# Kernel optimization log

Hardware: AMD Instinct MI355X
Metric: run time of the kernel (lower is better)

Reference implementation:

```python
import jax, jax.numpy as jnp
import numpy as np

E = 16       # num_experts
TOP_K = 2
D = 1024     # emb_dim
H = 1024     # moe_hidden_dim
SH = 2048    # shared_expert_hidden_dim
B, S = 2, 2048
W_SCALE = 0.02  # realistic init scale for weights


def setup_inputs() -> dict:
    key = jax.random.key(0)
    ks = jax.random.split(key, 9)
    return {
        "x": jax.random.normal(ks[0], (B, S, D), jnp.float32),
        "gate_w": jax.random.normal(ks[1], (E, D), jnp.float32) * W_SCALE,
        "w_gate": jax.random.normal(ks[2], (E, H, D), jnp.float32) * W_SCALE,
        "w1": jax.random.normal(ks[3], (E, H, D), jnp.float32) * W_SCALE,
        "w2": jax.random.normal(ks[4], (E, D, H), jnp.float32) * W_SCALE,
        "shared_w_gate": jax.random.normal(ks[5], (SH, D), jnp.float32) * W_SCALE,
        "shared_w1": jax.random.normal(ks[6], (SH, D), jnp.float32) * W_SCALE,
        "shared_w2": jax.random.normal(ks[7], (D, SH), jnp.float32) * W_SCALE,
        "shared_gate_w": jax.random.normal(ks[8], (1, D), jnp.float32) * W_SCALE,
    }


def reference(x, gate_w, w_gate, w1, w2, shared_w_gate, shared_w1, shared_w2, shared_gate_w):
    b, s, d = x.shape
    x2d = x.reshape(-1, d)                       # [N, D]
    n = x2d.shape[0]

    # --- router ---
    logits = x2d @ gate_w.T                      # [N, E]
    probs = jax.nn.softmax(logits, axis=-1)
    topk_p, topk_i = jax.lax.top_k(probs, TOP_K)  # [N, K]
    topk_p = topk_p / jnp.sum(topk_p, axis=-1, keepdims=True)

    # combine weights per (token, expert): zero for non-selected experts
    comb = jnp.zeros((n, E), x2d.dtype).at[jnp.arange(n)[:, None], topk_i].add(topk_p)  # [N, E]

    # --- per-expert gated FFN, accumulated via scan (keeps peak memory at [N,H]) ---
    def step(acc, ws):
        wg, wa, wo, cw = ws                      # [H,D], [H,D], [D,H], [N]
        h = (x2d @ wa.T) * jax.nn.silu(x2d @ wg.T)   # [N, H]
        return acc + cw[:, None] * (h @ wo.T), None

    out, _ = jax.lax.scan(step, jnp.zeros_like(x2d), (w_gate, w1, w2, comb.T))

    # --- shared expert path ---
    sh = (x2d @ shared_w1.T) * jax.nn.silu(x2d @ shared_w_gate.T)  # [N, SH]
    shared_out = sh @ shared_w2.T                                  # [N, D]
    sg = jax.nn.sigmoid(x2d @ shared_gate_w.T)                     # [N, 1]
    out = out + sg * shared_out

    return out.reshape(b, s, d)
```

## Files before the change

### kernel.cpp

```cpp
#include <hip/hip_runtime.h>
#include <stdint.h>

#define E_    16
#define TOPK  2
#define D_    1024
#define H_    1024
#define SH_   2048
#define NTOK  4096
#define BK    32
#define NDESC 80
#define RTOK  16
#define NRBLK (NTOK / RTOK)
#define NSHUP (NTOK/128 * SH_/128)
#define NRTUP (NDESC * H_/128)
#define NSHDN (NTOK/128 * D_/128)
#define NRTDN (NDESC * D_/128)

typedef unsigned short u16;
typedef __attribute__((ext_vector_type(8))) __bf16 bf16x8;
typedef __attribute__((ext_vector_type(4))) float  f32x4;

struct CvtTable {
  const float* src[7];
  u16*         dst[7];
  int          start[8];
};

__device__ __forceinline__ u16 f2bf(float f) {
  union { float f; unsigned int u; } v; v.f = f;
  unsigned int u = v.u;
  return (u16)((u + 0x7fffu + ((u >> 16) & 1u)) >> 16);
}

__device__ __forceinline__ void gload16(const void* g, void* l) {
  __builtin_amdgcn_global_load_lds(
      (const __attribute__((address_space(1))) unsigned int*)g,
      (__attribute__((address_space(3))) unsigned int*)l, 16, 0, 0);
}

__device__ __forceinline__ int swz8(int b, int nb) {
  return (b & 7) * (nb >> 3) + (b >> 3);
}

__global__ __launch_bounds__(256) void cvtrouter_k(
    CvtTable ct,
    const float* __restrict__ x, const float* __restrict__ gate_w,
    const float* __restrict__ shared_gate_w,
    int* __restrict__ topk_e, float* __restrict__ topk_w,
    float* __restrict__ sg, int* __restrict__ counts) {
  __shared__ float xs[RTOK][132];
  __shared__ float lg[RTOK][16];
  __shared__ float sgp[RTOK][16];

  int b   = blockIdx.x;
  int tid = threadIdx.x;

  if (b >= NRBLK) {
    int cb = b - NRBLK;
    int s = 0;
    while (cb >= ct.start[s + 1]) s++;
    int i = (cb - ct.start[s]) * 256 + tid;
    float4 f = ((const float4*)ct.src[s])[i];
    ushort4 o; o.x = f2bf(f.x); o.y = f2bf(f.y); o.z = f2bf(f.z); o.w = f2bf(f.w);
    ((ushort4*)ct.dst[s])[i] = o;
    return;
  }

  int e   = tid >> 4;
  int tt  = tid & 15;
  int t0  = b * RTOK;

  float acc = 0.f, sga = 0.f;
  for (int c = 0; c < D_; c += 128) {
    __syncthreads();
    #pragma unroll
    for (int i = 0; i < 2; i++) {
      int f = i * 256 + tid;
      int r = f >> 5, c4 = f & 31;
      *(float4*)&xs[r][c4 * 4] =
          *(const float4*)&x[(size_t)(t0 + r) * D_ + c + c4 * 4];
    }
    __syncthreads();
    const float* gw = &gate_w[(size_t)e * D_ + c];
    #pragma unroll
    for (int d4 = 0; d4 < 32; d4++) {
      float4 g  = *(const float4*)&gw[d4 * 4];
      float4 xv = *(const float4*)&xs[tt][d4 * 4];
      acc += xv.x * g.x + xv.y * g.y + xv.z * g.z + xv.w * g.w;
    }
    #pragma unroll
    for (int j = 0; j < 8; j += 4) {
      float4 s2 = *(const float4*)&shared_gate_w[c + e * 8 + j];
      float4 xv = *(const float4*)&xs[tt][e * 8 + j];
      sga += xv.x * s2.x + xv.y * s2.y + xv.z * s2.z + xv.w * s2.w;
    }
  }
  lg[tt][e]  = acc;
  sgp[tt][e] = sga;
  __syncthreads();

  if (tid < RTOK) {
    int t = t0 + tid;
    float l[16];
    #pragma unroll
    for (int k = 0; k < 16; k++) l[k] = lg[tid][k];
    int i0 = 0; float l0 = l[0];
    for (int k = 1; k < 16; k++) if (l[k] > l0) { l0 = l[k]; i0 = k; }
    int i1 = -1; float l1 = -3.4e38f;
    for (int k = 0; k < 16; k++) if (k != i0 && l[k] > l1) { l1 = l[k]; i1 = k; }
    float w0 = 1.f / (1.f + expf(l1 - l0));
    float s = 0.f;
    #pragma unroll
    for (int k = 0; k < 16; k++) s += sgp[tid][k];
    topk_e[2*t] = i0; topk_e[2*t+1] = i1;
    topk_w[2*t] = w0; topk_w[2*t+1] = 1.f - w0;
    sg[t] = 1.f / (1.f + expf(-s));
    atomicAdd(&counts[i0], 1);
    atomicAdd(&counts[i1], 1);
  }
}

__global__ __launch_bounds__(256) void scan_scatter_k(
    const int* __restrict__ counts, int* __restrict__ offs,
    int* __restrict__ desc_e, int* __restrict__ desc_m,
    const int* __restrict__ topk_e, const float* __restrict__ topk_w,
    int* __restrict__ fill, int* __restrict__ tok_of, float* __restrict__ w_of) {
  if (threadIdx.x == 0) {
    int s = 0, n = 0;
    for (int e = 0; e < E_; e++) {
      offs[e] = s;
      for (int m0 = 0; m0 < counts[e]; m0 += 128) {
        desc_e[n] = e; desc_m[n] = m0; n++;
      }
      s += counts[e];
    }
    offs[E_] = s;
    for (; n < NDESC; n++) { desc_e[n] = -1; desc_m[n] = 0; }
  }
  __syncthreads();
  for (int t = threadIdx.x; t < NTOK; t += 256) {
    for (int k = 0; k < TOPK; k++) {
      int e = topk_e[2*t+k];
      int p = atomicAdd(&fill[e], 1);
      int slot = offs[e] + p;
      tok_of[slot] = t;
      w_of[slot]   = topk_w[2*t+k];
    }
  }
}

__global__ __launch_bounds__(256, 2) void up_merged(
    const u16* __restrict__ Xb,
    const u16* __restrict__ sWg, const u16* __restrict__ sW1, u16* __restrict__ sHout,
    const u16* __restrict__ rWg_all, const u16* __restrict__ rW1_all, u16* __restrict__ rHout,
    const int* __restrict__ tok_of,
    const int* __restrict__ offs, const int* __restrict__ counts,
    const int* __restrict__ desc_e, const int* __restrict__ desc_m) {
  int bid = blockIdx.x;
  const u16 *Wg, *W1; u16* Hout; int Hdim;
  int m0, cnt, pbase, n0;
  const int* tof;
  if (bid < NSHUP) {
    int l = swz8(bid, NSHUP);
    int bx = l >> 4, by = l & 15;
    m0 = bx * 128; cnt = NTOK; pbase = 0; tof = nullptr;
    Wg = sWg; W1 = sW1; Hout = sHout; Hdim = SH_;
    n0 = by * 128;
  } else {
    int r = bid - NSHUP;
    int l = swz8(r, NRTUP);
    int bx = l >> 3, by = l & 7;
    int e = desc_e[bx];
    if (e < 0) return;
    m0 = desc_m[bx]; cnt = counts[e]; pbase = offs[e]; tof = tok_of;
    Wg = rWg_all + (size_t)e * H_ * D_;
    W1 = rW1_all + (size_t)e * H_ * D_;
    Hout = rHout; Hdim = H_;
    n0 = by * 128;
  }

  __shared__ u16 smem[2 * 3 * 4096];

  int tid  = threadIdx.x;
  int lane = tid & 63, wave = tid >> 6;
  int wm = wave & 1, wn = wave >> 1;
  int l16 = lane & 15, quad = lane >> 4;

  int sr = wave * 16 + (lane >> 2);
  int sc = (lane & 3) * 8;

  int gm0 = m0 + sr;      if (gm0 >= cnt) gm0 = cnt - 1;
  int gm1 = m0 + sr + 64; if (gm1 >= cnt) gm1 = cnt - 1;
  int tok0 = tof ? tof[pbase + gm0] : gm0;
  int tok1 = tof ? tof[pbase + gm1] : gm1;
  const u16* pa0 = Xb + (size_t)tok0 * D_ + sc;
  const u16* pa1 = Xb + (size_t)tok1 * D_ + sc;
  const u16* pg0 = Wg + (size_t)(n0 + sr) * D_ + sc;
  const u16* pg1 = pg0 + (size_t)64 * D_;
  const u16* pu0 = W1 + (size_t)(n0 + sr) * D_ + sc;
  const u16* pu1 = pu0 + (size_t)64 * D_;

  int lbase = wave * 512;

  f32x4 accg[4][4], accu[4][4];
  f32x4 zero = {0.f, 0.f, 0.f, 0.f};
  #pragma unroll
  for (int i = 0; i < 4; i++)
    #pragma unroll
    for (int j = 0; j < 4; j++) { accg[i][j] = zero; accu[i][j] = zero; }

#define STAGE_UP(b) do {                                            \
    u16* s_ = smem + (b) * 12288 + lbase;                           \
    gload16(pa0, s_);        gload16(pa1, s_ + 2048);               \
    gload16(pg0, s_ + 4096); gload16(pg1, s_ + 6144);               \
    gload16(pu0, s_ + 8192); gload16(pu1, s_ + 10240);              \
    pa0 += BK; pa1 += BK; pg0 += BK; pg1 += BK; pu0 += BK; pu1 += BK; \
  } while (0)

  STAGE_UP(0);
  STAGE_UP(1);
  int buf = 0;
  const int nt = D_ / BK;

  for (int t = 0; t < nt; ++t) {
    if (t + 1 < nt) asm volatile("s_waitcnt vmcnt(6)" ::: "memory");
    else            asm volatile("s_waitcnt vmcnt(0)" ::: "memory");
    __builtin_amdgcn_s_barrier();
    __builtin_amdgcn_sched_barrier(0);

    const u16* base = smem + buf * 12288;
    bf16x8 af[4], gf[4], uf[4];
    #pragma unroll
    for (int i = 0; i < 4; i++) {
      af[i] = *(const bf16x8*)&base[(wm*64 + i*16 + l16)*BK + quad*8];
      gf[i] = *(const bf16x8*)&base[4096 + (wn*64 + i*16 + l16)*BK + quad*8];
      uf[i] = *(const bf16x8*)&base[8192 + (wn*64 + i*16 + l16)*BK + quad*8];
    }
    #pragma unroll
    for (int i = 0; i < 4; i++)
      #pragma unroll
      for (int j = 0; j < 4; j++) {
        accg[i][j] = __builtin_amdgcn_mfma_f32_16x16x32_bf16(af[i], gf[j], accg[i][j], 0, 0, 0);
        accu[i][j] = __builtin_amdgcn_mfma_f32_16x16x32_bf16(af[i], uf[j], accu[i][j], 0, 0, 0);
      }

    __builtin_amdgcn_sched_barrier(0);
    __builtin_amdgcn_s_barrier();
    if (t + 2 < nt) STAGE_UP(buf);
    buf ^= 1;
  }
#undef STAGE_UP

  #pragma unroll
  for (int i = 0; i < 4; i++) {
    #pragma unroll
    for (int r = 0; r < 4; r++) {
      int m = m0 + wm*64 + i*16 + quad*4 + r;
      if (m < cnt) {
        size_t prow = (size_t)(pbase + m) * Hdim;
        #pragma unroll
        for (int j = 0; j < 4; j++) {
          int n = n0 + wn*64 + j*16 + l16;
          float g = accg[i][j][r];
          float u = accu[i][j][r];
          Hout[prow + n] = f2bf(u * (g / (1.f + expf(-g))));
        }
      }
    }
  }
}

__global__ __launch_bounds__(256, 3) void down_merged(
    const u16* __restrict__ sHbuf, const u16* __restrict__ sW2, const float* __restrict__ sg,
    const u16* __restrict__ rHbuf, const u16* __restrict__ rW2_all, const float* __restrict__ w_of,
    float* __restrict__ out,
    const int* __restrict__ tok_of,
    const int* __restrict__ offs, const int* __restrict__ counts,
    const int* __restrict__ desc_e, const int* __restrict__ desc_m) {
  int bid = blockIdx.x;
  const u16 *Hbuf, *W2; const float* scale;
  int m0, cnt, pbase, n0, K;
  const int* tof;
  if (bid < NSHDN) {
    int l = swz8(bid, NSHDN);
    int bx = l >> 3, by = l & 7;
    m0 = bx * 128; cnt = NTOK; pbase = 0; tof = nullptr;
    Hbuf = sHbuf; W2 = sW2; scale = sg; K = SH_;
    n0 = by * 128;
  } else {
    int r = bid - NSHDN;
    int l = swz8(r, NRTDN);
    int bx = l >> 3, by = l & 7;
    int e = desc_e[bx];
    if (e < 0) return;
    m0 = desc_m[bx]; cnt = counts[e]; pbase = offs[e]; tof = tok_of;
    Hbuf = rHbuf; W2 = rW2_all + (size_t)e * D_ * H_; scale = w_of; K = H_;
    n0 = by * 128;
  }

  __shared__ u16 smem[2 * 2 * 4096];

  int tid  = threadIdx.x;
  int lane = tid & 63, wave = tid >> 6;
  int wm = wave & 1, wn = wave >> 1;
  int l16 = lane & 15, quad = lane >> 4;

  int sr = wave * 16 + (lane >> 2);
  int sc = (lane & 3) * 8;

  int gm0 = m0 + sr;      if (gm0 >= cnt) gm0 = cnt - 1;
  int gm1 = m0 + sr + 64; if (gm1 >= cnt) gm1 = cnt - 1;
  const u16* pa0 = Hbuf + (size_t)(pbase + gm0) * K + sc;
  const u16* pa1 = Hbuf + (size_t)(pbase + gm1) * K + sc;
  const u16* pb0 = W2 + (size_t)(n0 + sr) * K + sc;
  const u16* pb1 = pb0 + (size_t)64 * K;

  int lbase = wave * 512;

  f32x4 acc[4][4];
  f32x4 zero = {0.f, 0.f, 0.f, 0.f};
  #pragma unroll
  for (int i = 0; i < 4; i++)
    #pragma unroll
    for (int j = 0; j < 4; j++) acc[i][j] = zero;

#define STAGE_DN(b) do {                                \
    u16* s_ = smem + (b) * 8192 + lbase;                \
    gload16(pa0, s_);        gload16(pa1, s_ + 2048);   \
    gload16(pb0, s_ + 4096); gload16(pb1, s_ + 6144);   \
    pa0 += BK; pa1 += BK; pb0 += BK; pb1 += BK;         \
  } while (0)

  STAGE_DN(0);
  STAGE_DN(1);
  int buf = 0;
  const int nt = K / BK;

  for (int t = 0; t < nt; ++t) {
    if (t + 1 < nt) asm volatile("s_waitcnt vmcnt(4)" ::: "memory");
    else            asm volatile("s_waitcnt vmcnt(0)" ::: "memory");
    __builtin_amdgcn_s_barrier();
    __builtin_amdgcn_sched_barrier(0);

    const u16* base = smem + buf * 8192;
    bf16x8 af[4], bfr[4];
    #pragma unroll
    for (int i = 0; i < 4; i++) {
      af[i]  = *(const bf16x8*)&base[(wm*64 + i*16 + l16)*BK + quad*8];
      bfr[i] = *(const bf16x8*)&base[4096 + (wn*64 + i*16 + l16)*BK + quad*8];
    }
    #pragma unroll
    for (int i = 0; i < 4; i++)
      #pragma unroll
      for (int j = 0; j < 4; j++)
        acc[i][j] = __builtin_amdgcn_mfma_f32_16x16x32_bf16(af[i], bfr[j], acc[i][j], 0, 0, 0);

    __builtin_amdgcn_sched_barrier(0);
    __builtin_amdgcn_s_barrier();
    if (t + 2 < nt) STAGE_DN(buf);
    buf ^= 1;
  }
#undef STAGE_DN

  #pragma unroll
  for (int i = 0; i < 4; i++) {
    #pragma unroll
    for (int r = 0; r < 4; r++) {
      int m = m0 + wm*64 + i*16 + quad*4 + r;
      if (m < cnt) {
        int p   = pbase + m;
        int tok = tof ? tof[p] : p;
        float sc2 = scale[p];
        #pragma unroll
        for (int j = 0; j < 4; j++) {
          int n = n0 + wn*64 + j*16 + l16;
          atomicAdd(&out[(size_t)tok * D_ + n], sc2 * acc[i][j][r]);
        }
      }
    }
  }
}

extern "C" void kernel_launch(void* const* d_in, const int* in_sizes, int n_in,
                              void* d_out, int out_size, void* d_ws, size_t ws_size,
                              hipStream_t stream) {
  const float* x      = (const float*)d_in[0];
  const float* gate_w = (const float*)d_in[1];
  const float* w_gate = (const float*)d_in[2];
  const float* w1     = (const float*)d_in[3];
  const float* w2     = (const float*)d_in[4];
  const float* sh_wg  = (const float*)d_in[5];
  const float* sh_w1  = (const float*)d_in[6];
  const float* sh_w2  = (const float*)d_in[7];
  const float* sh_gw  = (const float*)d_in[8];
  float* out = (float*)d_out;

  char* ws = (char*)d_ws;
  size_t off = 0;
  u16* xb    = (u16*)(ws + off); off += (size_t)NTOK * D_ * 2;
  u16* h_exp = (u16*)(ws + off); off += (size_t)NTOK * TOPK * H_ * 2;
  u16* h_sh  = (u16*)(ws + off); off += (size_t)NTOK * SH_ * 2;
  u16* wb_g  = (u16*)(ws + off); off += (size_t)E_ * H_ * D_ * 2;
  u16* wb_1  = (u16*)(ws + off); off += (size_t)E_ * H_ * D_ * 2;
  u16* wb_2  = (u16*)(ws + off); off += (size_t)E_ * D_ * H_ * 2;
  u16* sb_g  = (u16*)(ws + off); off += (size_t)SH_ * D_ * 2;
  u16* sb_1  = (u16*)(ws + off); off += (size_t)SH_ * D_ * 2;
  u16* sb_2  = (u16*)(ws + off); off += (size_t)D_ * SH_ * 2;
  int*   tok_of = (int*)  (ws + off); off += NTOK * TOPK * 4;
  float* w_of   = (float*)(ws + off); off += NTOK * TOPK * 4;
  float* sg     = (float*)(ws + off); off += NTOK * 4;
  int*   topk_e = (int*)  (ws + off); off += NTOK * TOPK * 4;
  float* topk_w = (float*)(ws + off); off += NTOK * TOPK * 4;
  int*   counts = (int*)  (ws + off); off += 64;
  int*   offs   = (int*)  (ws + off); off += 128;
  int*   fill   = (int*)  (ws + off); off += 64;
  int*   desc_e = (int*)  (ws + off); off += NDESC * 4;
  int*   desc_m = (int*)  (ws + off); off += NDESC * 4;

  hipMemsetAsync(counts, 0, 256, stream);
  hipMemsetAsync(out, 0, (size_t)NTOK * D_ * 4, stream);

  CvtTable ct;
  const float* srcs[7] = {x, w_gate, w1, w2, sh_wg, sh_w1, sh_w2};
  u16*         dsts[7] = {xb, wb_g, wb_1, wb_2, sb_g, sb_1, sb_2};
  int          nblk[7] = {NTOK*D_/1024, E_*H_*D_/1024, E_*H_*D_/1024,
                          E_*D_*H_/1024, SH_*D_/1024, SH_*D_/1024, D_*SH_/1024};
  int s = 0;
  for (int i = 0; i < 7; i++) { ct.src[i] = srcs[i]; ct.dst[i] = dsts[i];
                                ct.start[i] = s; s += nblk[i]; }
  ct.start[7] = s;

  cvtrouter_k<<<dim3(NRBLK + s), 256, 0, stream>>>(
      ct, x, gate_w, sh_gw, topk_e, topk_w, sg, counts);
  scan_scatter_k<<<dim3(1), 256, 0, stream>>>(
      counts, offs, desc_e, desc_m, topk_e, topk_w, fill, tok_of, w_of);

  up_merged<<<dim3(NSHUP + NRTUP), 256, 0, stream>>>(
      xb, sb_g, sb_1, h_sh, wb_g, wb_1, h_exp,
      tok_of, offs, counts, desc_e, desc_m);
  down_merged<<<dim3(NSHDN + NRTDN), 256, 0, stream>>>(
      h_sh, sb_2, sg, h_exp, wb_2, w_of, out,
      tok_of, offs, counts, desc_e, desc_m);

  (void)in_sizes; (void)n_in; (void)ws_size;
}
```

Baseline: 464.6 us.

## Defer down-proj weight conversion into up GEMM grid; atomic-free scatter

Moves the fp32-to-bf16 conversion of w2 and shared_w2 out of the first kernel and into extra tail blocks of the up-projection launch. The conversion then runs alongside the up GEMM instead of sitting on the critical path before it. Separately, replaces the global atomic counters and fill counters with a per-thread shared-memory histogram and prefix scan inside the single-block scatter kernel, which also removes the counts memset. The risk is that the conversion blocks compete with GEMM blocks for bandwidth and CUs, and that the scan serializes work on 16 threads.

```diff
diff --git a/kernel.cpp b/kernel.cpp
--- a/kernel.cpp
+++ b/kernel.cpp
@@ -15,15 +15,21 @@
 #define NRTUP (NDESC * H_/128)
 #define NSHDN (NTOK/128 * D_/128)
 #define NRTDN (NDESC * D_/128)
+#define NUPGEMM (NSHUP + NRTUP)
+#define NW2F4  (E_*D_*H_/4)
+#define NS2F4  (D_*SH_/4)
+#define CVT2W2 (NW2F4/4096)
+#define CVT2S2 (NS2F4/4096)
+#define NCVT2  (CVT2W2 + CVT2S2)
 
 typedef unsigned short u16;
 typedef __attribute__((ext_vector_type(8))) __bf16 bf16x8;
 typedef __attribute__((ext_vector_type(4))) float  f32x4;
 
 struct CvtTable {
-  const float* src[7];
-  u16*         dst[7];
-  int          start[8];
+  const float* src[5];
+  u16*         dst[5];
+  int          start[6];
 };
 
 __device__ __forceinline__ u16 f2bf(float f) {
@@ -47,7 +53,7 @@
     const float* __restrict__ x, const float* __restrict__ gate_w,
     const float* __restrict__ shared_gate_w,
     int* __restrict__ topk_e, float* __restrict__ topk_w,
-    float* __restrict__ sg, int* __restrict__ counts) {
+    float* __restrict__ sg) {
   __shared__ float xs[RTOK][132];
   __shared__ float lg[RTOK][16];
   __shared__ float sgp[RTOK][16];
@@ -115,33 +121,53 @@
     topk_e[2*t] = i0; topk_e[2*t+1] = i1;
     topk_w[2*t] = w0; topk_w[2*t+1] = 1.f - w0;
     sg[t] = 1.f / (1.f + expf(-s));
-    atomicAdd(&counts[i0], 1);
-    atomicAdd(&counts[i1], 1);
   }
 }
 
 __global__ __launch_bounds__(256) void scan_scatter_k(
-    const int* __restrict__ counts, int* __restrict__ offs,
+    const int* __restrict__ topk_e, const float* __restrict__ topk_w,
+    int* __restrict__ counts, int* __restrict__ offs,
     int* __restrict__ desc_e, int* __restrict__ desc_m,
-    const int* __restrict__ topk_e, const float* __restrict__ topk_w,
-    int* __restrict__ fill, int* __restrict__ tok_of, float* __restrict__ w_of) {
-  if (threadIdx.x == 0) {
+    int* __restrict__ tok_of, float* __restrict__ w_of) {
+  __shared__ int hc[256][E_];
+  __shared__ int etot[E_];
+  int tid = threadIdx.x;
+  #pragma unroll
+  for (int e = 0; e < E_; e++) hc[tid][e] = 0;
+  __syncthreads();
+
+  for (int i = 0; i < 16; i++) {
+    int t = tid * 16 + i;
+    hc[tid][topk_e[2*t]]++;
+    hc[tid][topk_e[2*t+1]]++;
+  }
+  __syncthreads();
+
+  if (tid < E_) {
+    int run = 0;
+    for (int k = 0; k < 256; k++) { int c = hc[k][tid]; hc[k][tid] = run; run += c; }
+    etot[tid] = run;
+  }
+  __syncthreads();
+
+  if (tid == 0) {
     int s = 0, n = 0;
     for (int e = 0; e < E_; e++) {
-      offs[e] = s;
-      for (int m0 = 0; m0 < counts[e]; m0 += 128) {
-        desc_e[n] = e; desc_m[n] = m0; n++;
-      }
-      s += counts[e];
+      offs[e] = s; counts[e] = etot[e];
+      for (int m0 = 0; m0 < etot[e]; m0 += 128) { desc_e[n] = e; desc_m[n] = m0; n++; }
+      s += etot[e];
     }
     offs[E_] = s;
     for (; n < NDESC; n++) { desc_e[n] = -1; desc_m[n] = 0; }
   }
   __syncthreads();
-  for (int t = threadIdx.x; t < NTOK; t += 256) {
+
+  for (int i = 0; i < 16; i++) {
+    int t = tid * 16 + i;
+    #pragma unroll
     for (int k = 0; k < TOPK; k++) {
       int e = topk_e[2*t+k];
-      int p = atomicAdd(&fill[e], 1);
+      int p = hc[tid][e]++;
       int slot = offs[e] + p;
       tok_of[slot] = t;
       w_of[slot]   = topk_w[2*t+k];
@@ -153,10 +179,28 @@
     const u16* __restrict__ Xb,
     const u16* __restrict__ sWg, const u16* __restrict__ sW1, u16* __restrict__ sHout,
     const u16* __restrict__ rWg_all, const u16* __restrict__ rW1_all, u16* __restrict__ rHout,
+    const float* __restrict__ w2f, u16* __restrict__ wb2,
+    const float* __restrict__ s2f, u16* __restrict__ sb2,
     const int* __restrict__ tok_of,
     const int* __restrict__ offs, const int* __restrict__ counts,
     const int* __restrict__ desc_e, const int* __restrict__ desc_m) {
   int bid = blockIdx.x;
+  if (bid >= NUPGEMM) {
+    int cb = bid - NUPGEMM;
+    const float4* src; ushort4* dst; int base;
+    if (cb < CVT2W2) { src = (const float4*)w2f; dst = (ushort4*)wb2; base = cb * 4096; }
+    else             { src = (const float4*)s2f; dst = (ushort4*)sb2; base = (cb - CVT2W2) * 4096; }
+    int tid = threadIdx.x;
+    #pragma unroll
+    for (int i = 0; i < 16; i++) {
+      int idx = base + i * 256 + tid;
+      float4 f = src[idx];
+      ushort4 o; o.x = f2bf(f.x); o.y = f2bf(f.y); o.z = f2bf(f.z); o.w = f2bf(f.w);
+      dst[idx] = o;
+    }
+    return;
+  }
+
   const u16 *Wg, *W1; u16* Hout; int Hdim;
   int m0, cnt, pbase, n0;
   const int* tof;
@@ -417,30 +461,30 @@
   int*   desc_e = (int*)  (ws + off); off += NDESC * 4;
   int*   desc_m = (int*)  (ws + off); off += NDESC * 4;
 
-  hipMemsetAsync(counts, 0, 256, stream);
   hipMemsetAsync(out, 0, (size_t)NTOK * D_ * 4, stream);
 
   CvtTable ct;
-  const float* srcs[7] = {x, w_gate, w1, w2, sh_wg, sh_w1, sh_w2};
-  u16*         dsts[7] = {xb, wb_g, wb_1, wb_2, sb_g, sb_1, sb_2};
-  int          nblk[7] = {NTOK*D_/1024, E_*H_*D_/1024, E_*H_*D_/1024,
-                          E_*D_*H_/1024, SH_*D_/1024, SH_*D_/1024, D_*SH_/1024};
+  const float* srcs[5] = {x, w_gate, w1, sh_wg, sh_w1};
+  u16*         dsts[5] = {xb, wb_g, wb_1, sb_g, sb_1};
+  int          nblk[5] = {NTOK*D_/1024, E_*H_*D_/1024, E_*H_*D_/1024,
+                          SH_*D_/1024, SH_*D_/1024};
   int s = 0;
-  for (int i = 0; i < 7; i++) { ct.src[i] = srcs[i]; ct.dst[i] = dsts[i];
+  for (int i = 0; i < 5; i++) { ct.src[i] = srcs[i]; ct.dst[i] = dsts[i];
                                 ct.start[i] = s; s += nblk[i]; }
-  ct.start[7] = s;
+  ct.start[5] = s;
 
   cvtrouter_k<<<dim3(NRBLK + s), 256, 0, stream>>>(
-      ct, x, gate_w, sh_gw, topk_e, topk_w, sg, counts);
+      ct, x, gate_w, sh_gw, topk_e, topk_w, sg);
   scan_scatter_k<<<dim3(1), 256, 0, stream>>>(
-      counts, offs, desc_e, desc_m, topk_e, topk_w, fill, tok_of, w_of);
-
-  up_merged<<<dim3(NSHUP + NRTUP), 256, 0, stream>>>(
+      topk_e, topk_w, counts, offs, desc_e, desc_m, tok_of, w_of);
+
+  up_merged<<<dim3(NUPGEMM + NCVT2), 256, 0, stream>>>(
       xb, sb_g, sb_1, h_sh, wb_g, wb_1, h_exp,
+      w2, wb_2, sh_w2, sb_2,
       tok_of, offs, counts, desc_e, desc_m);
   down_merged<<<dim3(NSHDN + NRTDN), 256, 0, stream>>>(
       h_sh, sb_2, sg, h_exp, wb_2, w_of, out,
       tok_of, offs, counts, desc_e, desc_m);
 
-  (void)in_sizes; (void)n_in; (void)ws_size;
-}
+  (void)in_sizes; (void)n_in; (void)ws_size; (void)fill;
+}
```

New measurement: 423.2 us. 1.1x faster.
